# Kernel optimization log

Hardware: AMD Instinct MI355X
Metric: run time of the kernel (lower is better)

Reference implementation:

```python
import jax, jax.numpy as jnp
import numpy as np

N = 2_000_000  # number of poses
EPS_THETA = 1e-6  # small-angle threshold from original module


def setup_inputs() -> dict:
    key = jax.random.key(0)
    k1, k2 = jax.random.split(key)
    xi = jax.random.normal(k1, (N, 6), dtype=jnp.float32) * 0.1  # (n,6) lie-algebra params
    poses_init = jax.random.normal(k2, (N, 4, 4), dtype=jnp.float32)  # (n,4,4) initial poses
    return {"xi": xi, "poses_init": poses_init}


def _skew(v):
    # v: (n,3) -> (n,3,3) skew-symmetric matrices
    z = jnp.zeros_like(v[..., 0])
    return jnp.stack([
        jnp.stack([z, -v[..., 2], v[..., 1]], axis=-1),
        jnp.stack([v[..., 2], z, -v[..., 0]], axis=-1),
        jnp.stack([-v[..., 1], v[..., 0], z], axis=-1),
    ], axis=-2)


def reference(xi, poses_init):
    # xi: (n,6) = [translation t (3), rotation omega (3)]
    t = xi[:, :3]
    omega = xi[:, 3:]
    theta = jnp.linalg.norm(omega, axis=-1)            # (n,)
    small = theta < EPS_THETA
    safe_theta = jnp.where(small, jnp.ones_like(theta), theta)
    k = omega / safe_theta[:, None]                    # unit axis
    K = _skew(k)                                       # (n,3,3)
    I3 = jnp.eye(3, dtype=xi.dtype)
    s = jnp.sin(theta)[:, None, None]
    c = (1.0 - jnp.cos(theta))[:, None, None]
    R_rod = I3 + s * K + c * jnp.einsum('nij,njk->nik', K, K)
    R_small = I3 + _skew(omega)                        # first-order branch as in original
    R = jnp.where(small[:, None, None], R_small, R_rod)  # (n,3,3)

    # assemble (n,4,4) homogeneous transform [[R, t], [0, 1]]
    top = jnp.concatenate([R, t[:, :, None]], axis=-1)               # (n,3,4)
    bottom_row = jnp.array([0.0, 0.0, 0.0, 1.0], dtype=xi.dtype)
    bottom = jnp.broadcast_to(bottom_row, (xi.shape[0], 1, 4))
    T = jnp.concatenate([top, bottom], axis=1)                       # (n,4,4)

    # right-multiply by initial poses: delta @ pose_init
    return jnp.einsum('nij,njk->nik', T, poses_init)
```

## Files before the change

### kernel.cpp

```cpp
#include <hip/hip_runtime.h>
#include <hip/hip_bf16.h>

#define EPS_THETA 1e-6f

__device__ __forceinline__ float4 shfl4(float4 v, int src) {
    float4 r;
    r.x = __shfl(v.x, src, 4);
    r.y = __shfl(v.y, src, 4);
    r.z = __shfl(v.z, src, 4);
    r.w = __shfl(v.w, src, 4);
    return r;
}

__global__ __launch_bounds__(256) void se3_compose_kernel(
    const float* __restrict__ xi,
    const float4* __restrict__ poses4,
    float4* __restrict__ out4,
    int n4)
{
    int i = blockIdx.x * blockDim.x + threadIdx.x;
    if (i >= n4) return;

    int p = i >> 2;
    int r = i & 3;

    const float2* x2 = (const float2*)(xi + 6ll * p);
    float2 a  = x2[0];
    float2 b  = x2[1];
    float2 cc = x2[2];
    float t0 = a.x, t1 = a.y, t2 = b.x;
    float w0 = b.y, w1 = cc.x, w2 = cc.y;

    float4 pr = poses4[i];

    float theta2 = w0 * w0 + w1 * w1 + w2 * w2;
    float theta  = sqrtf(theta2);
    bool  small_ = theta < EPS_THETA;

    float inv = small_ ? 1.0f : (1.0f / theta);
    float k0 = w0 * inv, k1 = w1 * inv, k2 = w2 * inv;

    float s = small_ ? 1.0f : sinf(theta);
    float c = small_ ? 0.0f : (1.0f - cosf(theta));

    float R00 = 1.0f + c * (k0 * k0 - 1.0f);
    float R01 = c * k0 * k1 - s * k2;
    float R02 = c * k0 * k2 + s * k1;
    float R10 = c * k0 * k1 + s * k2;
    float R11 = 1.0f + c * (k1 * k1 - 1.0f);
    float R12 = c * k1 * k2 - s * k0;
    float R20 = c * k0 * k2 - s * k1;
    float R21 = c * k1 * k2 + s * k0;
    float R22 = 1.0f + c * (k2 * k2 - 1.0f);

    float c0 = (r == 0) ? R00 : (r == 1) ? R10 : (r == 2) ? R20 : 0.0f;
    float c1 = (r == 0) ? R01 : (r == 1) ? R11 : (r == 2) ? R21 : 0.0f;
    float c2 = (r == 0) ? R02 : (r == 1) ? R12 : (r == 2) ? R22 : 0.0f;
    float c3 = (r == 0) ? t0  : (r == 1) ? t1  : (r == 2) ? t2  : 1.0f;

    float4 P0 = shfl4(pr, 0);
    float4 P1 = shfl4(pr, 1);
    float4 P2 = shfl4(pr, 2);
    float4 P3 = shfl4(pr, 3);

    float4 o;
    o.x = c0 * P0.x + c1 * P1.x + c2 * P2.x + c3 * P3.x;
    o.y = c0 * P0.y + c1 * P1.y + c2 * P2.y + c3 * P3.y;
    o.z = c0 * P0.z + c1 * P1.z + c2 * P2.z + c3 * P3.z;
    o.w = c0 * P0.w + c1 * P1.w + c2 * P2.w + c3 * P3.w;

    out4[i] = o;
}

extern "C" void kernel_launch(void* const* d_in, const int* in_sizes, int n_in,
                              void* d_out, int out_size, void* d_ws, size_t ws_size,
                              hipStream_t stream) {
    const float*  xi     = (const float*)d_in[0];
    const float4* poses4 = (const float4*)d_in[1];
    float4*       out4   = (float4*)d_out;

    int n  = in_sizes[0] / 6;
    int n4 = 4 * n;

    const int block = 256;
    const int grid  = (n4 + block - 1) / block;
    se3_compose_kernel<<<grid, block, 0, stream>>>(xi, poses4, out4, n4);
}
```

Baseline: 248.0 us.

## Process one pose per thread with polynomial Rodrigues and nontemporal stores

Each thread now handles a whole pose instead of one output row. It loads all four pose rows directly, which removes the cross-lane shuffles and the redundant per-row recomputation of the rotation. The sin/cos of theta are replaced by Taylor series for sin(x)/x and (1-cos x)/x² when theta is below 1.5, with the exact formula as a fallback above that. Outputs are written with nontemporal stores. The trade-off is a strided 64-byte per-thread access pattern that coalesces less well. The small-angle branch also differs slightly from the reference's first-order approximation, but within tolerance.

Result: slower. 340.3 us (+37.2%).

```diff
diff --git a/kernel.cpp b/kernel.cpp
--- a/kernel.cpp
+++ b/kernel.cpp
@@ -1,28 +1,20 @@
 #include <hip/hip_runtime.h>
-#include <hip/hip_bf16.h>
 
-#define EPS_THETA 1e-6f
+typedef float fx4 __attribute__((ext_vector_type(4)));
 
-__device__ __forceinline__ float4 shfl4(float4 v, int src) {
-    float4 r;
-    r.x = __shfl(v.x, src, 4);
-    r.y = __shfl(v.y, src, 4);
-    r.z = __shfl(v.z, src, 4);
-    r.w = __shfl(v.w, src, 4);
-    return r;
+__device__ __forceinline__ void nt_store4(float4* p, float4 v) {
+    fx4 vv = {v.x, v.y, v.z, v.w};
+    __builtin_nontemporal_store(vv, (fx4*)p);
 }
 
 __global__ __launch_bounds__(256) void se3_compose_kernel(
     const float* __restrict__ xi,
     const float4* __restrict__ poses4,
     float4* __restrict__ out4,
-    int n4)
+    int n)
 {
-    int i = blockIdx.x * blockDim.x + threadIdx.x;
-    if (i >= n4) return;
-
-    int p = i >> 2;
-    int r = i & 3;
+    int p = blockIdx.x * blockDim.x + threadIdx.x;
+    if (p >= n) return;
 
     const float2* x2 = (const float2*)(xi + 6ll * p);
     float2 a  = x2[0];
@@ -31,45 +23,56 @@
     float t0 = a.x, t1 = a.y, t2 = b.x;
     float w0 = b.y, w1 = cc.x, w2 = cc.y;
 
-    float4 pr = poses4[i];
+    const float4* P = poses4 + 4ll * p;
+    float4 P0 = P[0];
+    float4 P1 = P[1];
+    float4 P2 = P[2];
+    float4 P3 = P[3];
 
-    float theta2 = w0 * w0 + w1 * w1 + w2 * w2;
-    float theta  = sqrtf(theta2);
-    bool  small_ = theta < EPS_THETA;
+    float x = w0 * w0 + w1 * w1 + w2 * w2;
+    float A, B;
+    if (__builtin_expect(x < 2.25f, 1)) {
+        A = 1.0f + x * (-1.0f / 6.0f   + x * (1.0f / 120.0f  + x * (-1.0f / 5040.0f  + x * (1.0f / 362880.0f))));
+        B = 0.5f + x * (-1.0f / 24.0f  + x * (1.0f / 720.0f  + x * (-1.0f / 40320.0f + x * (1.0f / 3628800.0f))));
+    } else {
+        float th = sqrtf(x);
+        float s  = sinf(th);
+        float c  = cosf(th);
+        A = s / th;
+        B = (1.0f - c) / x;
+    }
 
-    float inv = small_ ? 1.0f : (1.0f / theta);
-    float k0 = w0 * inv, k1 = w1 * inv, k2 = w2 * inv;
+    float w00 = w0 * w0, w11 = w1 * w1, w22 = w2 * w2;
+    float R00 = 1.0f - B * (w11 + w22);
+    float R11 = 1.0f - B * (w00 + w22);
+    float R22 = 1.0f - B * (w00 + w11);
+    float Bw01 = B * (w0 * w1), Bw02 = B * (w0 * w2), Bw12 = B * (w1 * w2);
+    float Aw0 = A * w0, Aw1 = A * w1, Aw2 = A * w2;
+    float R01 = Bw01 - Aw2, R10 = Bw01 + Aw2;
+    float R02 = Bw02 + Aw1, R20 = Bw02 - Aw1;
+    float R12 = Bw12 - Aw0, R21 = Bw12 + Aw0;
 
-    float s = small_ ? 1.0f : sinf(theta);
-    float c = small_ ? 0.0f : (1.0f - cosf(theta));
+    float4 o0, o1, o2;
+    o0.x = R00 * P0.x + R01 * P1.x + R02 * P2.x + t0 * P3.x;
+    o0.y = R00 * P0.y + R01 * P1.y + R02 * P2.y + t0 * P3.y;
+    o0.z = R00 * P0.z + R01 * P1.z + R02 * P2.z + t0 * P3.z;
+    o0.w = R00 * P0.w + R01 * P1.w + R02 * P2.w + t0 * P3.w;
 
-    float R00 = 1.0f + c * (k0 * k0 - 1.0f);
-    float R01 = c * k0 * k1 - s * k2;
-    float R02 = c * k0 * k2 + s * k1;
-    float R10 = c * k0 * k1 + s * k2;
-    float R11 = 1.0f + c * (k1 * k1 - 1.0f);
-    float R12 = c * k1 * k2 - s * k0;
-    float R20 = c * k0 * k2 - s * k1;
-    float R21 = c * k1 * k2 + s * k0;
-    float R22 = 1.0f + c * (k2 * k2 - 1.0f);
+    o1.x = R10 * P0.x + R11 * P1.x + R12 * P2.x + t1 * P3.x;
+    o1.y = R10 * P0.y + R11 * P1.y + R12 * P2.y + t1 * P3.y;
+    o1.z = R10 * P0.z + R11 * P1.z + R12 * P2.z + t1 * P3.z;
+    o1.w = R10 * P0.w + R11 * P1.w + R12 * P2.w + t1 * P3.w;
 
-    float c0 = (r == 0) ? R00 : (r == 1) ? R10 : (r == 2) ? R20 : 0.0f;
-    float c1 = (r == 0) ? R01 : (r == 1) ? R11 : (r == 2) ? R21 : 0.0f;
-    float c2 = (r == 0) ? R02 : (r == 1) ? R12 : (r == 2) ? R22 : 0.0f;
-    float c3 = (r == 0) ? t0  : (r == 1) ? t1  : (r == 2) ? t2  : 1.0f;
+    o2.x = R20 * P0.x + R21 * P1.x + R22 * P2.x + t2 * P3.x;
+    o2.y = R20 * P0.y + R21 * P1.y + R22 * P2.y + t2 * P3.y;
+    o2.z = R20 * P0.z + R21 * P1.z + R22 * P2.z + t2 * P3.z;
+    o2.w = R20 * P0.w + R21 * P1.w + R22 * P2.w + t2 * P3.w;
 
-    float4 P0 = shfl4(pr, 0);
-    float4 P1 = shfl4(pr, 1);
-    float4 P2 = shfl4(pr, 2);
-    float4 P3 = shfl4(pr, 3);
-
-    float4 o;
-    o.x = c0 * P0.x + c1 * P1.x + c2 * P2.x + c3 * P3.x;
-    o.y = c0 * P0.y + c1 * P1.y + c2 * P2.y + c3 * P3.y;
-    o.z = c0 * P0.z + c1 * P1.z + c2 * P2.z + c3 * P3.z;
-    o.w = c0 * P0.w + c1 * P1.w + c2 * P2.w + c3 * P3.w;
-
-    out4[i] = o;
+    float4* O = out4 + 4ll * p;
+    nt_store4(O + 0, o0);
+    nt_store4(O + 1, o1);
+    nt_store4(O + 2, o2);
+    nt_store4(O + 3, P3);
 }
 
 extern "C" void kernel_launch(void* const* d_in, const int* in_sizes, int n_in,
@@ -79,10 +82,9 @@
     const float4* poses4 = (const float4*)d_in[1];
     float4*       out4   = (float4*)d_out;
 
-    int n  = in_sizes[0] / 6;
-    int n4 = 4 * n;
+    int n = in_sizes[0] / 6;
 
     const int block = 256;
-    const int grid  = (n4 + block - 1) / block;
-    se3_compose_kernel<<<grid, block, 0, stream>>>(xi, poses4, out4, n4);
+    const int grid  = (n + block - 1) / block;
+    se3_compose_kernel<<<grid, block, 0, stream>>>(xi, poses4, out4, n);
 }
```

## Use Taylor-series Rodrigues coefficients, DPP quad permutes, and nontemporal stores

Applied to the files above, without the earlier changes.

Rewrites the Rodrigues rotation using the coefficients A=sin(θ)/θ and B=(1-cos θ)/θ², evaluated by polynomial series for small angles. This avoids the sqrt, divide and sin/cos on the common path. Each lane now computes only its own row through a rotated-index formulation, and quad-wide shuffles become DPP permutes. Output is written with nontemporal stores. The kernel is memory-bound, so reducing compute may matter little; the small-angle branch also differs slightly from the reference's first-order branch for θ<1e-6.

After: 249.1 us. Within noise of the previous version (+0.4%).

```diff
diff --git a/kernel.cpp b/kernel.cpp
--- a/kernel.cpp
+++ b/kernel.cpp
@@ -1,16 +1,30 @@
 #include <hip/hip_runtime.h>
-#include <hip/hip_bf16.h>
 
-#define EPS_THETA 1e-6f
+typedef float fx4 __attribute__((ext_vector_type(4)));
 
-__device__ __forceinline__ float4 shfl4(float4 v, int src) {
+__device__ __forceinline__ void nt_store4(float4* p, float4 v) {
+    fx4 vv = {v.x, v.y, v.z, v.w};
+    __builtin_nontemporal_store(vv, (fx4*)p);
+}
+
+template<int CTRL>
+__device__ __forceinline__ float qperm(float v) {
+    return __int_as_float(__builtin_amdgcn_update_dpp(
+        0, __float_as_int(v), CTRL, 0xF, 0xF, true));
+}
+template<int CTRL>
+__device__ __forceinline__ float4 qperm4(float4 v) {
     float4 r;
-    r.x = __shfl(v.x, src, 4);
-    r.y = __shfl(v.y, src, 4);
-    r.z = __shfl(v.z, src, 4);
-    r.w = __shfl(v.w, src, 4);
+    r.x = qperm<CTRL>(v.x);
+    r.y = qperm<CTRL>(v.y);
+    r.z = qperm<CTRL>(v.z);
+    r.w = qperm<CTRL>(v.w);
     return r;
 }
+
+#define ROT1 0xC9
+#define ROT2 0xD2
+#define BC3  0xFF
 
 __global__ __launch_bounds__(256) void se3_compose_kernel(
     const float* __restrict__ xi,
@@ -33,43 +47,39 @@
 
     float4 pr = poses4[i];
 
-    float theta2 = w0 * w0 + w1 * w1 + w2 * w2;
-    float theta  = sqrtf(theta2);
-    bool  small_ = theta < EPS_THETA;
+    float x = w0 * w0 + w1 * w1 + w2 * w2;
+    float A, B;
+    if (__builtin_expect(x < 2.25f, 1)) {
+        A = 1.0f + x * (-1.0f / 6.0f  + x * (1.0f / 120.0f + x * (-1.0f / 5040.0f  + x * (1.0f / 362880.0f))));
+        B = 0.5f + x * (-1.0f / 24.0f + x * (1.0f / 720.0f + x * (-1.0f / 40320.0f + x * (1.0f / 3628800.0f))));
+    } else {
+        float th = sqrtf(x);
+        A = sinf(th) / th;
+        B = (1.0f - cosf(th)) / x;
+    }
 
-    float inv = small_ ? 1.0f : (1.0f / theta);
-    float k0 = w0 * inv, k1 = w1 * inv, k2 = w2 * inv;
+    float wr = (r == 0) ? w0 : (r == 1) ? w1 : w2;
+    float tr = (r == 0) ? t0 : (r == 1) ? t1 : (r == 2) ? t2 : 0.0f;
 
-    float s = small_ ? 1.0f : sinf(theta);
-    float c = small_ ? 0.0f : (1.0f - cosf(theta));
+    float wa = qperm<ROT1>(wr);
+    float wb = qperm<ROT2>(wr);
 
-    float R00 = 1.0f + c * (k0 * k0 - 1.0f);
-    float R01 = c * k0 * k1 - s * k2;
-    float R02 = c * k0 * k2 + s * k1;
-    float R10 = c * k0 * k1 + s * k2;
-    float R11 = 1.0f + c * (k1 * k1 - 1.0f);
-    float R12 = c * k1 * k2 - s * k0;
-    float R20 = c * k0 * k2 - s * k1;
-    float R21 = c * k1 * k2 + s * k0;
-    float R22 = 1.0f + c * (k2 * k2 - 1.0f);
+    float4 Pa = qperm4<ROT1>(pr);
+    float4 Pb = qperm4<ROT2>(pr);
+    float4 P3 = qperm4<BC3>(pr);
 
-    float c0 = (r == 0) ? R00 : (r == 1) ? R10 : (r == 2) ? R20 : 0.0f;
-    float c1 = (r == 0) ? R01 : (r == 1) ? R11 : (r == 2) ? R21 : 0.0f;
-    float c2 = (r == 0) ? R02 : (r == 1) ? R12 : (r == 2) ? R22 : 0.0f;
-    float c3 = (r == 0) ? t0  : (r == 1) ? t1  : (r == 2) ? t2  : 1.0f;
-
-    float4 P0 = shfl4(pr, 0);
-    float4 P1 = shfl4(pr, 1);
-    float4 P2 = shfl4(pr, 2);
-    float4 P3 = shfl4(pr, 3);
+    float diag = 1.0f - B * (wa * wa + wb * wb);
+    float off1 = B * wr * wa - A * wb;
+    float off2 = B * wr * wb + A * wa;
+    if (r == 3) { diag = 1.0f; off1 = 0.0f; off2 = 0.0f; }
 
     float4 o;
-    o.x = c0 * P0.x + c1 * P1.x + c2 * P2.x + c3 * P3.x;
-    o.y = c0 * P0.y + c1 * P1.y + c2 * P2.y + c3 * P3.y;
-    o.z = c0 * P0.z + c1 * P1.z + c2 * P2.z + c3 * P3.z;
-    o.w = c0 * P0.w + c1 * P1.w + c2 * P2.w + c3 * P3.w;
+    o.x = diag * pr.x + off1 * Pa.x + off2 * Pb.x + tr * P3.x;
+    o.y = diag * pr.y + off1 * Pa.y + off2 * Pb.y + tr * P3.y;
+    o.z = diag * pr.z + off1 * Pa.z + off2 * Pb.z + tr * P3.z;
+    o.w = diag * pr.w + off1 * Pa.w + off2 * Pb.w + tr * P3.w;
 
-    out4[i] = o;
+    nt_store4(&out4[i], o);
 }
 
 extern "C" void kernel_launch(void* const* d_in, const int* in_sizes, int n_in,
```
